# Kernel optimization log

Hardware: AMD Instinct MI355X
Metric: run time of the kernel (lower is better)

The kernel has to match this reference:

```python
import jax, jax.numpy as jnp
import numpy as np

B, S, D, H, E = 2, 2048, 1024, 4096, 8


def setup_inputs() -> dict:
    key = jax.random.key(0)
    k0, k1, k2, k3 = jax.random.split(key, 4)
    x = jax.random.normal(k0, (B, S, D), dtype=jnp.float32)
    router_w = jax.random.normal(k1, (E, D), dtype=jnp.float32) * 0.02   # Top2Router Linear weight [E, D]
    w1 = jax.random.normal(k2, (E, D, H), dtype=jnp.float32) * 0.02      # stacked fc1 weights (transposed: x @ w1[e])
    w2 = jax.random.normal(k3, (E, H, D), dtype=jnp.float32) * 0.02      # stacked fc2 weights
    return {"x": x, "router_w": router_w, "w1": w1, "w2": w2}


def reference(x, router_w, w1, w2):
    # x: [B, S, D] -> flatten tokens. Single-rank EP: all-to-all is identity,
    # microbatch split is a pure overlap trick, per-token math unchanged.
    b, s, d = x.shape
    e = router_w.shape[0]
    xf = x.reshape(-1, d)                                     # [T, D]
    # Top-2 router with renormalized gate weights
    probs = jax.nn.softmax(xf @ router_w.T, axis=-1)          # [T, E]
    topv, topi = jax.lax.top_k(probs, 2)                      # [T, 2]
    topv = topv / (topv.sum(axis=-1, keepdims=True) + 1e-9)
    # Combine weights per expert: cw[t,e] = sum_k topv[t,k] * [topi[t,k]==e]
    cw = (jax.nn.one_hot(topi, e, dtype=xf.dtype) * topv[..., None]).sum(axis=1)  # [T, E]
    # Expert MLPs (dense-over-experts reference for the grouped GEMM)
    h = jax.nn.gelu(jnp.einsum('td,edh->teh', xf, w1), approximate=False)  # [T, E, H]
    y = jnp.einsum('teh,ehd->ted', h, w2)                                   # [T, E, D]
    out = jnp.einsum('te,ted->td', cw, y)                                   # weighted combine (scatter-add equiv.)
    return out.reshape(b, s, d)
```

## Files before the change

### kernel.cpp

```cpp
#include <hip/hip_runtime.h>

#define T_TOK 4096
#define DIM   1024
#define HID   4096
#define NEXP  8

typedef unsigned short u16;
typedef __attribute__((ext_vector_type(8))) short short8;
typedef __attribute__((ext_vector_type(4))) float f32x4;
typedef __attribute__((ext_vector_type(4))) unsigned short u16x4;

typedef __attribute__((address_space(3))) unsigned int lds_uint;
typedef const __attribute__((address_space(1))) unsigned int gbl_uint;

__device__ __forceinline__ u16 f2bf(float f) {
    union { float f; unsigned int u; } v; v.f = f;
    unsigned int r = v.u + 0x7fffu + ((v.u >> 16) & 1u);
    return (u16)(r >> 16);
}

__global__ __launch_bounds__(256)
void transpose_cast(const float* __restrict__ in, u16* __restrict__ out, int R, int C) {
    __shared__ float tile[32][33];
    size_t mo = (size_t)blockIdx.z * R * C;
    const float* ip = in + mo;
    u16* op = out + mo;
    int c0 = blockIdx.x * 32, r0 = blockIdx.y * 32;
    int tx = threadIdx.x, ty = threadIdx.y;
#pragma unroll
    for (int i = 0; i < 4; ++i)
        tile[ty + 8*i][tx] = ip[(size_t)(r0 + ty + 8*i) * C + c0 + tx];
    __syncthreads();
#pragma unroll
    for (int i = 0; i < 4; ++i)
        op[(size_t)(c0 + ty + 8*i) * R + r0 + tx] = f2bf(tile[tx][ty + 8*i]);
}

__global__ __launch_bounds__(256)
void router_k(const float* __restrict__ x, const float* __restrict__ rw,
              int* __restrict__ counts, int* __restrict__ tE,
              int* __restrict__ tS, float* __restrict__ tG) {
    int wave = threadIdx.x >> 6, lane = threadIdx.x & 63;
    int t = blockIdx.x * 4 + wave;
    const float* xr = x + (size_t)t * DIM;
    float xv[16];
#pragma unroll
    for (int i = 0; i < 16; ++i) xv[i] = xr[lane + 64*i];
    float lg[NEXP];
#pragma unroll
    for (int e = 0; e < NEXP; ++e) {
        const float* wr_ = rw + e * DIM;
        float a = 0.f;
#pragma unroll
        for (int i = 0; i < 16; ++i) a += xv[i] * wr_[lane + 64*i];
        lg[e] = a;
    }
#pragma unroll
    for (int off = 32; off > 0; off >>= 1)
#pragma unroll
        for (int e = 0; e < NEXP; ++e) lg[e] += __shfl_xor(lg[e], off, 64);
    if (lane == 0) {
        float mx = lg[0];
        for (int e = 1; e < NEXP; ++e) mx = fmaxf(mx, lg[e]);
        float p[NEXP], s = 0.f;
        for (int e = 0; e < NEXP; ++e) { p[e] = expf(lg[e] - mx); s += p[e]; }
        float inv_s = 1.f / s;
        for (int e = 0; e < NEXP; ++e) p[e] *= inv_s;
        int i0 = 0;
        for (int e = 1; e < NEXP; ++e) if (p[e] > p[i0]) i0 = e;
        int i1 = (i0 == 0) ? 1 : 0;
        for (int e = 0; e < NEXP; ++e) if (e != i0 && p[e] > p[i1]) i1 = e;
        float v0 = p[i0], v1 = p[i1];
        float inv = 1.f / (v0 + v1 + 1e-9f);
        int s0 = atomicAdd(&counts[i0], 1);
        int s1 = atomicAdd(&counts[i1], 1);
        tE[2*t] = i0;  tE[2*t+1] = i1;
        tS[2*t] = s0;  tS[2*t+1] = s1;
        tG[2*t] = v0 * inv;  tG[2*t+1] = v1 * inv;
    }
}

__global__ void scan_k(const int* __restrict__ counts, int* __restrict__ pbase) {
    if (threadIdx.x == 0) {
        int o = 0;
        for (int e = 0; e < NEXP; ++e) { pbase[e] = o; o += ((counts[e] + 127) >> 7) << 7; }
        pbase[NEXP] = o;
    }
}

__global__ __launch_bounds__(256)
void gather_k(const float* __restrict__ x, const int* __restrict__ tE,
              const int* __restrict__ tS, const int* __restrict__ pbase,
              u16* __restrict__ xg) {
    int a = blockIdx.x;
    int t = a >> 1, k = a & 1;
    int e = tE[2*t + k];
    int row = pbase[e] + tS[2*t + k];
    const f32x4* xr = (const f32x4*)(x + (size_t)t * DIM);
    u16x4* o = (u16x4*)(xg + (size_t)row * DIM);
    int i = threadIdx.x;
    f32x4 v = xr[i];
    u16x4 r; r.x = f2bf(v.x); r.y = f2bf(v.y); r.z = f2bf(v.z); r.w = f2bf(v.w);
    o[i] = r;
}

template<int K, bool GELU, typename OutT>
__global__ __launch_bounds__(256)
void gemm_bt(const u16* __restrict__ A, const u16* __restrict__ BtAll,
             OutT* __restrict__ C, const int* __restrict__ counts,
             const int* __restrict__ pbase, int N) {
    int e = blockIdx.z;
    int cnt = counts[e];
    int mt = blockIdx.y;
    if (mt * 128 >= cnt) return;
    const u16* Bt = BtAll + (size_t)e * N * K;
    int row0 = pbase[e] + mt * 128;
    int col0 = blockIdx.x * 128;

    __shared__ __align__(16) u16 As[128 * 64];
    __shared__ __align__(16) u16 Bs[128 * 64];

    int tid = threadIdx.x;
    int lane = tid & 63;
    int w = tid >> 6;
    int quad = lane >> 4, m16 = lane & 15;
    int wr = (w >> 1) * 64, wc = (w & 1) * 64;
    int rsub = lane >> 3;
    int kch  = lane & 7;

    f32x4 acc[4][4] = {};

    for (int kb = 0; kb < K; kb += 64) {
#pragma unroll
        for (int i = 0; i < 4; ++i) {
            int grp = w * 4 + i;
            int r = grp * 8 + rsub;
            const u16* ga = A + (size_t)(row0 + r) * K + kb + kch * 8;
            __builtin_amdgcn_global_load_lds((gbl_uint*)ga, (lds_uint*)(As + grp * 512), 16, 0, 0);
            const u16* gb = Bt + (size_t)(col0 + r) * K + kb + kch * 8;
            __builtin_amdgcn_global_load_lds((gbl_uint*)gb, (lds_uint*)(Bs + grp * 512), 16, 0, 0);
        }
        __syncthreads();
#pragma unroll
        for (int ks = 0; ks < 64; ks += 32) {
            short8 af[4], bfr[4];
#pragma unroll
            for (int mi = 0; mi < 4; ++mi)
                af[mi] = *(const short8*)(As + (wr + mi * 16 + m16) * 64 + ks + quad * 8);
#pragma unroll
            for (int ni = 0; ni < 4; ++ni)
                bfr[ni] = *(const short8*)(Bs + (wc + ni * 16 + m16) * 64 + ks + quad * 8);
#pragma unroll
            for (int mi = 0; mi < 4; ++mi)
#pragma unroll
                for (int ni = 0; ni < 4; ++ni)
                    acc[mi][ni] = __builtin_amdgcn_mfma_f32_16x16x32_bf16(af[mi], bfr[ni], acc[mi][ni], 0, 0, 0);
        }
        __syncthreads();
    }

#pragma unroll
    for (int mi = 0; mi < 4; ++mi) {
#pragma unroll
        for (int r = 0; r < 4; ++r) {
            int mrow = wr + mi * 16 + quad * 4 + r;
            size_t rowoff = (size_t)(row0 + mrow) * N + col0;
#pragma unroll
            for (int ni = 0; ni < 4; ++ni) {
                int ncol = wc + ni * 16 + m16;
                float v = acc[mi][ni][r];
                if (GELU) {
                    float g = 0.5f * v * (1.0f + erff(v * 0.70710678118f));
                    ((u16*)C)[rowoff + ncol] = f2bf(g);
                } else {
                    ((float*)C)[rowoff + ncol] = v;
                }
            }
        }
    }
}

__global__ __launch_bounds__(256)
void combine_k(const float* __restrict__ yb, const int* __restrict__ tE,
               const int* __restrict__ tS, const float* __restrict__ tG,
               const int* __restrict__ pbase, float* __restrict__ out) {
    int t = blockIdx.x;
    int e0 = tE[2*t], e1 = tE[2*t+1];
    int r0 = pbase[e0] + tS[2*t];
    int r1 = pbase[e1] + tS[2*t+1];
    float g0 = tG[2*t], g1 = tG[2*t+1];
    const f32x4* y0 = (const f32x4*)(yb + (size_t)r0 * DIM);
    const f32x4* y1 = (const f32x4*)(yb + (size_t)r1 * DIM);
    f32x4* o = (f32x4*)(out + (size_t)t * DIM);
    int i = threadIdx.x;
    o[i] = g0 * y0[i] + g1 * y1[i];
}

extern "C" void kernel_launch(void* const* d_in, const int* in_sizes, int n_in,
                              void* d_out, int out_size, void* d_ws, size_t ws_size,
                              hipStream_t stream) {
    const float* x  = (const float*)d_in[0];
    const float* rw = (const float*)d_in[1];
    const float* w1 = (const float*)d_in[2];
    const float* w2 = (const float*)d_in[3];
    float* out = (float*)d_out;

    char* ws = (char*)d_ws;
    u16* w1t = (u16*)(ws + 0);
    u16* w2t = (u16*)(ws + 67108864ull);
    u16* xg  = (u16*)(ws + 134217728ull);
    u16* hb  = (u16*)(ws + 153092096ull);
    float* yb = (float*)(ws + 0);
    int* ctrl   = (int*)(ws + 228589568ull);
    int* counts = ctrl;
    int* pbase  = ctrl + 8;
    int* tE     = ctrl + 32;
    int* tS     = ctrl + 32 + 8192;
    float* tG   = (float*)(ctrl + 32 + 16384);

    hipMemsetAsync(counts, 0, 8 * sizeof(int), stream);

    transpose_cast<<<dim3(128, 32, NEXP), dim3(32, 8), 0, stream>>>(w1, w1t, DIM, HID);
    transpose_cast<<<dim3(32, 128, NEXP), dim3(32, 8), 0, stream>>>(w2, w2t, HID, DIM);
    router_k<<<T_TOK / 4, 256, 0, stream>>>(x, rw, counts, tE, tS, tG);
    scan_k<<<1, 64, 0, stream>>>(counts, pbase);
    gather_k<<<T_TOK * 2, 256, 0, stream>>>(x, tE, tS, pbase, xg);
    gemm_bt<DIM, true, u16><<<dim3(HID / 128, 32, NEXP), 256, 0, stream>>>(xg, w1t, hb, counts, pbase, HID);
    gemm_bt<HID, false, float><<<dim3(DIM / 128, 32, NEXP), 256, 0, stream>>>(hb, w2t, yb, counts, pbase, DIM);
    combine_k<<<T_TOK, 256, 0, stream>>>(yb, tE, tS, tG, pbase, out);
}
```

Measured before the change: 778.9 us.

## Split-K second expert GEMM, vectorize transpose, stage GELU epilogue through LDS

Several changes land together. The weight transpose-cast now uses 64x64 tiles with vector loads and stores. The first GEMM's epilogue uses a tanh-form GELU via exp and writes bf16 output through a swizzled LDS tile for coalesced 16-byte stores. The second GEMM is split two ways along K into two partial buffers that combine_k sums, which doubles the block count for that GEMM to improve occupancy. The costs are approximating erf-GELU with the tanh form and the extra partial-buffer traffic in combine.

```diff
diff --git a/kernel.cpp b/kernel.cpp
--- a/kernel.cpp
+++ b/kernel.cpp
@@ -4,11 +4,13 @@
 #define DIM   1024
 #define HID   4096
 #define NEXP  8
+#define MAXROWS 9216
 
 typedef unsigned short u16;
 typedef __attribute__((ext_vector_type(8))) short short8;
 typedef __attribute__((ext_vector_type(4))) float f32x4;
 typedef __attribute__((ext_vector_type(4))) unsigned short u16x4;
+typedef __attribute__((ext_vector_type(8))) unsigned short u16x8;
 
 typedef __attribute__((address_space(3))) unsigned int lds_uint;
 typedef const __attribute__((address_space(1))) unsigned int gbl_uint;
@@ -19,21 +21,40 @@
     return (u16)(r >> 16);
 }
 
+__device__ __forceinline__ float gelu_f(float v) {
+    float u = 1.5957691216f * (v + 0.044715f * v * v * v);
+    float s = 1.0f / (1.0f + __expf(-u));
+    return v * s;
+}
+
 __global__ __launch_bounds__(256)
 void transpose_cast(const float* __restrict__ in, u16* __restrict__ out, int R, int C) {
-    __shared__ float tile[32][33];
+    __shared__ u16 t[64 * 68];
     size_t mo = (size_t)blockIdx.z * R * C;
     const float* ip = in + mo;
     u16* op = out + mo;
-    int c0 = blockIdx.x * 32, r0 = blockIdx.y * 32;
-    int tx = threadIdx.x, ty = threadIdx.y;
-#pragma unroll
-    for (int i = 0; i < 4; ++i)
-        tile[ty + 8*i][tx] = ip[(size_t)(r0 + ty + 8*i) * C + c0 + tx];
+    int c0 = blockIdx.x * 64, r0 = blockIdx.y * 64;
+    int tid = threadIdx.x;
+#pragma unroll
+    for (int j = 0; j < 4; ++j) {
+        int id = tid + 256 * j;
+        int r = id >> 4, cc = id & 15;
+        f32x4 v = *(const f32x4*)(ip + (size_t)(r0 + r) * C + c0 + 4 * cc);
+        u16x4 w; w.x = f2bf(v.x); w.y = f2bf(v.y); w.z = f2bf(v.z); w.w = f2bf(v.w);
+        *(u16x4*)(t + r * 68 + 4 * cc) = w;
+    }
     __syncthreads();
 #pragma unroll
-    for (int i = 0; i < 4; ++i)
-        op[(size_t)(c0 + ty + 8*i) * R + r0 + tx] = f2bf(tile[tx][ty + 8*i]);
+    for (int j = 0; j < 4; ++j) {
+        int id = tid + 256 * j;
+        int c = id >> 4, rj = id & 15;
+        u16x4 o;
+        o.x = t[(4 * rj + 0) * 68 + c];
+        o.y = t[(4 * rj + 1) * 68 + c];
+        o.z = t[(4 * rj + 2) * 68 + c];
+        o.w = t[(4 * rj + 3) * 68 + c];
+        *(u16x4*)(op + (size_t)(c0 + c) * R + r0 + 4 * rj) = o;
+    }
 }
 
 __global__ __launch_bounds__(256)
@@ -104,21 +125,26 @@
     o[i] = r;
 }
 
-template<int K, bool GELU, typename OutT>
+template<int K, int KSPLIT, bool GELU, typename OutT>
 __global__ __launch_bounds__(256)
 void gemm_bt(const u16* __restrict__ A, const u16* __restrict__ BtAll,
              OutT* __restrict__ C, const int* __restrict__ counts,
-             const int* __restrict__ pbase, int N) {
-    int e = blockIdx.z;
+             const int* __restrict__ pbase, int N, size_t cstride) {
+    int e  = blockIdx.z / KSPLIT;
+    int ks = blockIdx.z % KSPLIT;
     int cnt = counts[e];
     int mt = blockIdx.y;
     if (mt * 128 >= cnt) return;
     const u16* Bt = BtAll + (size_t)e * N * K;
+    OutT* Cp = C + (size_t)ks * cstride;
     int row0 = pbase[e] + mt * 128;
     int col0 = blockIdx.x * 128;
-
-    __shared__ __align__(16) u16 As[128 * 64];
-    __shared__ __align__(16) u16 Bs[128 * 64];
+    const int kb0 = ks * (K / KSPLIT);
+    const int kb1 = kb0 + (K / KSPLIT);
+
+    __shared__ __align__(16) u16 smem[128 * 128];
+    u16* As = smem;
+    u16* Bs = smem + 128 * 64;
 
     int tid = threadIdx.x;
     int lane = tid & 63;
@@ -130,7 +156,7 @@
 
     f32x4 acc[4][4] = {};
 
-    for (int kb = 0; kb < K; kb += 64) {
+    for (int kb = kb0; kb < kb1; kb += 64) {
 #pragma unroll
         for (int i = 0; i < 4; ++i) {
             int grp = w * 4 + i;
@@ -142,14 +168,14 @@
         }
         __syncthreads();
 #pragma unroll
-        for (int ks = 0; ks < 64; ks += 32) {
+        for (int ks2 = 0; ks2 < 64; ks2 += 32) {
             short8 af[4], bfr[4];
 #pragma unroll
             for (int mi = 0; mi < 4; ++mi)
-                af[mi] = *(const short8*)(As + (wr + mi * 16 + m16) * 64 + ks + quad * 8);
+                af[mi] = *(const short8*)(As + (wr + mi * 16 + m16) * 64 + ks2 + quad * 8);
 #pragma unroll
             for (int ni = 0; ni < 4; ++ni)
-                bfr[ni] = *(const short8*)(Bs + (wc + ni * 16 + m16) * 64 + ks + quad * 8);
+                bfr[ni] = *(const short8*)(Bs + (wc + ni * 16 + m16) * 64 + ks2 + quad * 8);
 #pragma unroll
             for (int mi = 0; mi < 4; ++mi)
 #pragma unroll
@@ -159,41 +185,62 @@
         __syncthreads();
     }
 
-#pragma unroll
-    for (int mi = 0; mi < 4; ++mi) {
-#pragma unroll
-        for (int r = 0; r < 4; ++r) {
-            int mrow = wr + mi * 16 + quad * 4 + r;
-            size_t rowoff = (size_t)(row0 + mrow) * N + col0;
-#pragma unroll
-            for (int ni = 0; ni < 4; ++ni) {
-                int ncol = wc + ni * 16 + m16;
-                float v = acc[mi][ni][r];
-                if (GELU) {
-                    float g = 0.5f * v * (1.0f + erff(v * 0.70710678118f));
-                    ((u16*)C)[rowoff + ncol] = f2bf(g);
-                } else {
-                    ((float*)C)[rowoff + ncol] = v;
+    if (GELU) {
+#pragma unroll
+        for (int mi = 0; mi < 4; ++mi) {
+#pragma unroll
+            for (int r = 0; r < 4; ++r) {
+                int row = wr + mi * 16 + quad * 4 + r;
+#pragma unroll
+                for (int ni = 0; ni < 4; ++ni) {
+                    int col = wc + ni * 16 + m16;
+                    int c16 = col >> 3, w8 = col & 7;
+                    smem[row * 128 + (((c16 ^ (row & 15)) << 3) | w8)] = f2bf(gelu_f(acc[mi][ni][r]));
                 }
             }
         }
-    }
-}
-
-__global__ __launch_bounds__(256)
-void combine_k(const float* __restrict__ yb, const int* __restrict__ tE,
-               const int* __restrict__ tS, const float* __restrict__ tG,
-               const int* __restrict__ pbase, float* __restrict__ out) {
+        __syncthreads();
+#pragma unroll
+        for (int j = 0; j < 8; ++j) {
+            int id = tid + 256 * j;
+            int row = id >> 4, c16 = id & 15;
+            u16x8 val = *(const u16x8*)(smem + row * 128 + ((c16 ^ (row & 15)) << 3));
+            *(u16x8*)((u16*)Cp + (size_t)(row0 + row) * N + col0 + c16 * 8) = val;
+        }
+    } else {
+#pragma unroll
+        for (int mi = 0; mi < 4; ++mi) {
+#pragma unroll
+            for (int r = 0; r < 4; ++r) {
+                int mrow = wr + mi * 16 + quad * 4 + r;
+                size_t rowoff = (size_t)(row0 + mrow) * N + col0;
+#pragma unroll
+                for (int ni = 0; ni < 4; ++ni) {
+                    int ncol = wc + ni * 16 + m16;
+                    ((float*)Cp)[rowoff + ncol] = acc[mi][ni][r];
+                }
+            }
+        }
+    }
+}
+
+__global__ __launch_bounds__(256)
+void combine_k(const float* __restrict__ p0, const float* __restrict__ p1,
+               const int* __restrict__ tE, const int* __restrict__ tS,
+               const float* __restrict__ tG, const int* __restrict__ pbase,
+               float* __restrict__ out) {
     int t = blockIdx.x;
     int e0 = tE[2*t], e1 = tE[2*t+1];
     int r0 = pbase[e0] + tS[2*t];
     int r1 = pbase[e1] + tS[2*t+1];
     float g0 = tG[2*t], g1 = tG[2*t+1];
-    const f32x4* y0 = (const f32x4*)(yb + (size_t)r0 * DIM);
-    const f32x4* y1 = (const f32x4*)(yb + (size_t)r1 * DIM);
+    int i = threadIdx.x;
+    f32x4 a0 = ((const f32x4*)(p0 + (size_t)r0 * DIM))[i];
+    f32x4 b0 = ((const f32x4*)(p1 + (size_t)r0 * DIM))[i];
+    f32x4 a1 = ((const f32x4*)(p0 + (size_t)r1 * DIM))[i];
+    f32x4 b1 = ((const f32x4*)(p1 + (size_t)r1 * DIM))[i];
     f32x4* o = (f32x4*)(out + (size_t)t * DIM);
-    int i = threadIdx.x;
-    o[i] = g0 * y0[i] + g1 * y1[i];
+    o[i] = g0 * (a0 + b0) + g1 * (a1 + b1);
 }
 
 extern "C" void kernel_launch(void* const* d_in, const int* in_sizes, int n_in,
@@ -207,10 +254,11 @@
 
     char* ws = (char*)d_ws;
     u16* w1t = (u16*)(ws + 0);
-    u16* w2t = (u16*)(ws + 67108864ull);
-    u16* xg  = (u16*)(ws + 134217728ull);
+    u16* xg  = (u16*)(ws + 67108864ull);
+    u16* w2t = (u16*)(ws + 85983232ull);
     u16* hb  = (u16*)(ws + 153092096ull);
-    float* yb = (float*)(ws + 0);
+    float* p0 = (float*)(ws + 0);
+    float* p1 = (float*)(ws + 37748736ull);
     int* ctrl   = (int*)(ws + 228589568ull);
     int* counts = ctrl;
     int* pbase  = ctrl + 8;
@@ -220,12 +268,14 @@
 
     hipMemsetAsync(counts, 0, 8 * sizeof(int), stream);
 
-    transpose_cast<<<dim3(128, 32, NEXP), dim3(32, 8), 0, stream>>>(w1, w1t, DIM, HID);
-    transpose_cast<<<dim3(32, 128, NEXP), dim3(32, 8), 0, stream>>>(w2, w2t, HID, DIM);
+    transpose_cast<<<dim3(HID / 64, DIM / 64, NEXP), 256, 0, stream>>>(w1, w1t, DIM, HID);
+    transpose_cast<<<dim3(DIM / 64, HID / 64, NEXP), 256, 0, stream>>>(w2, w2t, HID, DIM);
     router_k<<<T_TOK / 4, 256, 0, stream>>>(x, rw, counts, tE, tS, tG);
     scan_k<<<1, 64, 0, stream>>>(counts, pbase);
     gather_k<<<T_TOK * 2, 256, 0, stream>>>(x, tE, tS, pbase, xg);
-    gemm_bt<DIM, true, u16><<<dim3(HID / 128, 32, NEXP), 256, 0, stream>>>(xg, w1t, hb, counts, pbase, HID);
-    gemm_bt<HID, false, float><<<dim3(DIM / 128, 32, NEXP), 256, 0, stream>>>(hb, w2t, yb, counts, pbase, DIM);
-    combine_k<<<T_TOK, 256, 0, stream>>>(yb, tE, tS, tG, pbase, out);
-}
+    gemm_bt<DIM, 1, true, u16><<<dim3(HID / 128, 32, NEXP), 256, 0, stream>>>(
+        xg, w1t, hb, counts, pbase, HID, 0);
+    gemm_bt<HID, 2, false, float><<<dim3(DIM / 128, 32, NEXP * 2), 256, 0, stream>>>(
+        hb, w2t, p0, counts, pbase, DIM, (size_t)MAXROWS * DIM);
+    combine_k<<<T_TOK, 256, 0, stream>>>(p0, p1, tE, tS, tG, pbase, out);
+}
```

New measurement: 735.9 us. 5.5% less time.
